# Optimization experiments

Hardware: AMD Instinct MI355X
Metric: run time of the kernel (lower is better)

## Reference

```python
import jax, jax.numpy as jnp
import numpy as np

B, L, H, NUM_VOCABS = 512, 64, 256, 2046
OUT = NUM_VOCABS + 2


def setup_inputs() -> dict:
    key = jax.random.key(0)
    k1, k2, k3 = jax.random.split(key, 3)
    mol_vec = jax.random.normal(k1, (B, L, H), jnp.float32)
    # parent of node t is a strictly earlier node in the same tree; root (t=0) has none
    rng = np.random.default_rng(0)
    pid = np.zeros((B, L), np.int32)
    for t in range(1, L):
        pid[:, t] = rng.integers(0, t, size=B)
    parent_idx = jnp.asarray(pid)
    Wp = jax.random.normal(k2, (H, H), jnp.float32) * (1.0 / np.sqrt(H))
    bp = jnp.zeros((H,), jnp.float32)
    Wc = jax.random.normal(k3, (H, OUT), jnp.float32) * (1.0 / np.sqrt(H))
    bc = jnp.zeros((OUT,), jnp.float32)
    return dict(mol_vec=mol_vec, parent_idx=parent_idx, Wp=Wp, bp=bp, Wc=Wc, bc=bc)


def _sibling_mean(mol_vec, parent_idx):
    # sibling edges connect nodes sharing a parent; message = mean of siblings' mol_vec
    b, l, h = mol_vec.shape
    seg = parent_idx + jnp.arange(b, dtype=parent_idx.dtype)[:, None] * l  # per-tree parent segment
    seg = jnp.where(jnp.arange(l)[None, :] == 0, b * l, seg)  # roots -> dummy segment
    seg_flat = seg.reshape(-1)
    mv_flat = mol_vec.reshape(-1, h)
    child_sum = jax.ops.segment_sum(mv_flat, seg_flat, num_segments=b * l + 1)
    child_cnt = jax.ops.segment_sum(jnp.ones((b * l,), mol_vec.dtype), seg_flat, num_segments=b * l + 1)
    sib_sum = child_sum[seg_flat] - mv_flat           # exclude self
    sib_cnt = child_cnt[seg_flat] - 1.0
    sib_mean = jnp.where(sib_cnt[:, None] > 0, sib_sum / jnp.maximum(sib_cnt, 1.0)[:, None], 0.0)
    sib_mean = sib_mean.reshape(b, l, h)
    # roots receive no sibling update (their dummy segment is meaningless)
    return jnp.where(jnp.arange(l)[None, :, None] == 0, 0.0, sib_mean)


def _forward(mol_vec, parent_idx, Wp, bp, Wc, bc):
    b, l, h = mol_vec.shape
    sib_mean = _sibling_mean(mol_vec, parent_idx)  # static: mol_vec does not depend on z
    batch_ar = jnp.arange(b)

    def body(z, t):
        # gather parent z (each node has exactly one parent edge; sum == gather)
        pz = z[batch_ar, parent_idx[:, t]]                     # [B, H]
        new = jax.nn.relu(pz @ Wp + bp) + sib_mean[:, t]       # parent_layer + sibling mean
        return z.at[:, t].set(new), None

    z0 = jnp.zeros((b, l, h), mol_vec.dtype)
    z, _ = jax.lax.scan(body, z0, jnp.arange(1, l))
    logits = z.reshape(-1, h) @ Wc + bc                         # classify_layer -> [N, V+2]
    return logits


def reference(mol_vec, parent_idx, Wp, bp, Wc, bc):
    return _forward(mol_vec, parent_idx, Wp, bp, Wc, bc)
```

## Files before the change

kernel.cpp:

```cpp
#include <hip/hip_runtime.h>

#define B_ 512
#define L_ 64
#define H_ 256
#define OUT_ 2048

typedef short bf16x8 __attribute__((ext_vector_type(8)));
typedef float f32x4 __attribute__((ext_vector_type(4)));

static __device__ __forceinline__ unsigned short f2bf(float f) {
  union { float f; unsigned int u; } v; v.f = f;
  unsigned int r = (v.u + 0x7FFFu + ((v.u >> 16) & 1u)) >> 16;
  return (unsigned short)r;
}
static __device__ __forceinline__ float bf2f(unsigned short s) {
  union { unsigned int u; float f; } v; v.u = ((unsigned int)s) << 16;
  return v.f;
}

__global__ __launch_bounds__(256) void pack_kernel(
    const float* __restrict__ Wc, const float* __restrict__ Wp,
    unsigned short* __restrict__ WcB, unsigned short* __restrict__ WpB) {
  int bid = blockIdx.x;
  const float* W;
  unsigned short* dst;
  int ncols, col16;
  if (bid < 128) { W = Wc; dst = WcB; ncols = OUT_; col16 = bid; }
  else           { W = Wp; dst = WpB; ncols = H_;   col16 = bid - 128; }
  int tid = threadIdx.x, l = tid & 63, q = tid >> 6;
  int n = col16 * 16 + (l & 15), g = l >> 4;
#pragma unroll
  for (int kk = 0; kk < 2; ++kk) {
    int kt = q + kk * 4;
    bf16x8 v;
#pragma unroll
    for (int i = 0; i < 8; ++i)
      v[i] = (short)f2bf(W[(size_t)(kt * 32 + g * 8 + i) * ncols + n]);
    *(bf16x8*)&dst[(size_t)(col16 * 8 + kt) * 512 + l * 8] = v;
  }
}

__global__ __launch_bounds__(256, 2) void fused_kernel(
    const float* __restrict__ mol, const int* __restrict__ pidx_g,
    const float* __restrict__ bp, const unsigned short* __restrict__ WpB,
    const unsigned short* __restrict__ WcB, const float* __restrict__ bc,
    float* __restrict__ out) {
  __shared__ unsigned short zbuf[65 * H_];
  __shared__ int pidx[L_];
  __shared__ int cnt_i[64];
  __shared__ unsigned short scale_s[64];
  __shared__ int lvlcnt[64];
  __shared__ int lvlbase[64];
  __shared__ int chkbase[64];
  __shared__ int order_s[64];
  __shared__ int cstart_s[64];
  __shared__ int ccnt_s[64];
  __shared__ int nchunks_s;

  int bid = blockIdx.x;
  int b = bid >> 1, half = bid & 1;
  int tid = threadIdx.x;
  int wv = tid >> 6, l = tid & 63, g = l >> 4, c = l & 15;

  if (tid < 64) pidx[tid] = pidx_g[b * L_ + tid];

  const float* molb = mol + (size_t)b * L_ * H_;
#pragma unroll
  for (int i = 0; i < 8; ++i) {
    int idx = tid + i * 256;
    int t = idx >> 5, h0 = (idx & 31) * 8;
    f32x4 lo = *(const f32x4*)&molb[t * H_ + h0];
    f32x4 hi = *(const f32x4*)&molb[t * H_ + h0 + 4];
    bf16x8 v;
#pragma unroll
    for (int q = 0; q < 4; ++q) { v[q] = (short)f2bf(lo[q]); v[q + 4] = (short)f2bf(hi[q]); }
    *(bf16x8*)&zbuf[(t * H_ + h0) ^ ((t & 7) << 3)] = v;
  }

  if (tid < 64) {
    int t = tid;
    cnt_i[t] = 0;
    lvlcnt[t] = 0;
    int pp = pidx[t];
    if (t >= 1) atomicAdd(&cnt_i[pp], 1);
    int lev = (t == 0) ? 0 : 1;
#pragma unroll
    for (int it = 0; it < 6; ++it) {
      int dp = __shfl(lev, pp);
      int pp2 = __shfl(pp, pp);
      lev += dp;
      pp = pp2;
    }
    int cc = (t >= 1) ? (cnt_i[pidx[t]] - 1) : 0;
    scale_s[t] = (t >= 1 && cc > 0) ? f2bf(1.f / (float)cc) : 0;
    int rank = 0;
    if (t >= 1) rank = atomicAdd(&lvlcnt[lev], 1);
    int lc = lvlcnt[t];
    int nchk = (lc + 15) >> 4;
    int offx = lc, chkx = nchk;
#pragma unroll
    for (int d = 1; d < 64; d <<= 1) {
      int u = __shfl_up(offx, d);
      int v2 = __shfl_up(chkx, d);
      if (t >= d) { offx += u; chkx += v2; }
    }
    lvlbase[t] = offx - lc;
    chkbase[t] = chkx - nchk;
    if (t == 63) nchunks_s = chkx;
    if (t >= 1) {
      int pos = lvlbase[lev] + rank;
      order_s[pos] = t;
      if ((rank & 15) == 0) {
        int cid = chkbase[lev] + (rank >> 4);
        cstart_s[cid] = pos;
        ccnt_s[cid] = min(16, lvlcnt[lev] - rank);
      }
    }
  }
  __syncthreads();

  {
    int pv[2][8];
#pragma unroll
    for (int kt = 0; kt < 2; ++kt)
#pragma unroll
      for (int i = 0; i < 8; ++i) pv[kt][i] = pidx[kt * 32 + g * 8 + i];
    bf16x8 bfr[4][2];
#pragma unroll
    for (int nt = 0; nt < 4; ++nt) {
      int tn = nt * 16 + c;
      int pt = pidx[tn];
      unsigned short scl = scale_s[tn];
#pragma unroll
      for (int kt = 0; kt < 2; ++kt) {
        bf16x8 bv;
#pragma unroll
        for (int i = 0; i < 8; ++i) {
          int tp = kt * 32 + g * 8 + i;
          bv[i] = (tp >= 1 && tp != tn && pv[kt][i] == pt) ? (short)scl : (short)0;
        }
        bfr[nt][kt] = bv;
      }
    }
#pragma unroll
    for (int mtl = 0; mtl < 4; ++mtl) {
      int mtg = wv * 4 + mtl;
      int colh = mtg * 16 + c;
      bf16x8 afr[2];
#pragma unroll
      for (int kt = 0; kt < 2; ++kt) {
        bf16x8 av;
#pragma unroll
        for (int i = 0; i < 8; ++i) {
          int tp = kt * 32 + g * 8 + i;
          av[i] = (short)zbuf[(tp * H_ + colh) ^ ((tp & 7) << 3)];
        }
        afr[kt] = av;
      }
      f32x4 acc4[4] = {};
#pragma unroll
      for (int nt = 0; nt < 4; ++nt)
#pragma unroll
        for (int kt = 0; kt < 2; ++kt)
          acc4[nt] = __builtin_amdgcn_mfma_f32_16x16x32_bf16(afr[kt], bfr[nt][kt], acc4[nt], 0, 0, 0);
#pragma unroll
      for (int nt = 0; nt < 4; ++nt) {
        int ts = nt * 16 + c;
        int swn = (ts & 7) << 3;
#pragma unroll
        for (int j = 0; j < 4; ++j) {
          int h = mtg * 16 + g * 4 + j;
          zbuf[(ts * H_ + h) ^ swn] = f2bf(acc4[nt][j]);
        }
      }
    }
  }

  bf16x8 wfr[4][8];
#pragma unroll
  for (int nt = 0; nt < 4; ++nt)
#pragma unroll
    for (int kt = 0; kt < 8; ++kt)
      wfr[nt][kt] = *(const bf16x8*)&WpB[(size_t)((wv * 4 + nt) * 8 + kt) * 512 + l * 8];
  float bpv[4];
#pragma unroll
  for (int nt = 0; nt < 4; ++nt) bpv[nt] = bp[wv * 64 + nt * 16 + c];
  __syncthreads();

  int nch = nchunks_s;
  for (int ch = 0; ch < nch; ++ch) {
    int cs = cstart_s[ch], cc = ccnt_s[ch];
    int node = (c < cc) ? order_s[cs + c] : 64;
    int par = (node < 64) ? pidx[node] : 0;
    int sp = (par & 7) << 3;
    f32x4 a0 = {0.f, 0.f, 0.f, 0.f};
    f32x4 a1 = {0.f, 0.f, 0.f, 0.f};
    f32x4 a2 = {0.f, 0.f, 0.f, 0.f};
    f32x4 a3 = {0.f, 0.f, 0.f, 0.f};
#pragma unroll
    for (int kt = 0; kt < 8; ++kt) {
      bf16x8 av = *(const bf16x8*)&zbuf[par * H_ + ((kt * 32 + g * 8) ^ sp)];
      a0 = __builtin_amdgcn_mfma_f32_16x16x32_bf16(av, wfr[0][kt], a0, 0, 0, 0);
      a1 = __builtin_amdgcn_mfma_f32_16x16x32_bf16(av, wfr[1][kt], a1, 0, 0, 0);
      a2 = __builtin_amdgcn_mfma_f32_16x16x32_bf16(av, wfr[2][kt], a2, 0, 0, 0);
      a3 = __builtin_amdgcn_mfma_f32_16x16x32_bf16(av, wfr[3][kt], a3, 0, 0, 0);
    }
#pragma unroll
    for (int j = 0; j < 4; ++j) {
      int m = g * 4 + j;
      int nd = (m < cc) ? order_s[cs + m] : 64;
      int swn = (nd & 7) << 3;
      int base = nd * H_ + wv * 64 + c;
      int i0 = (base + 0) ^ swn, i1 = (base + 16) ^ swn;
      int i2 = (base + 32) ^ swn, i3 = (base + 48) ^ swn;
      float v0 = fmaxf(a0[j] + bpv[0], 0.f) + bf2f(zbuf[i0]);
      float v1 = fmaxf(a1[j] + bpv[1], 0.f) + bf2f(zbuf[i1]);
      float v2 = fmaxf(a2[j] + bpv[2], 0.f) + bf2f(zbuf[i2]);
      float v3 = fmaxf(a3[j] + bpv[3], 0.f) + bf2f(zbuf[i3]);
      zbuf[i0] = f2bf(v0);
      zbuf[i1] = f2bf(v1);
      zbuf[i2] = f2bf(v2);
      zbuf[i3] = f2bf(v3);
    }
    __syncthreads();
  }

#pragma unroll 1
  for (int nc = 0; nc < 4; ++nc) {
    int colbase = half * 1024 + wv * 256 + nc * 64;
    float bcv[4];
#pragma unroll
    for (int nt = 0; nt < 4; ++nt) bcv[nt] = bc[colbase + nt * 16 + c];
    f32x4 acc[4][4] = {};
#pragma unroll
    for (int kt = 0; kt < 8; ++kt) {
      bf16x8 a[4], bfr[4];
#pragma unroll
      for (int mt = 0; mt < 4; ++mt) {
        int r = mt * 16 + c;
        a[mt] = *(const bf16x8*)&zbuf[r * H_ + ((kt * 32 + g * 8) ^ ((r & 7) << 3))];
      }
#pragma unroll
      for (int nt = 0; nt < 4; ++nt) {
        int col16 = (colbase >> 4) + nt;
        bfr[nt] = *(const bf16x8*)&WcB[(size_t)(col16 * 8 + kt) * 512 + l * 8];
      }
#pragma unroll
      for (int nt = 0; nt < 4; ++nt)
#pragma unroll
        for (int mt = 0; mt < 4; ++mt)
          acc[mt][nt] = __builtin_amdgcn_mfma_f32_16x16x32_bf16(
              a[mt], bfr[nt], acc[mt][nt], 0, 0, 0);
    }
#pragma unroll
    for (int mt = 0; mt < 4; ++mt)
#pragma unroll
      for (int nt = 0; nt < 4; ++nt) {
        int col = colbase + nt * 16 + c;
#pragma unroll
        for (int j = 0; j < 4; ++j) {
          int rt = mt * 16 + g * 4 + j;
          out[(size_t)(b * 64 + rt) * OUT_ + col] = acc[mt][nt][j] + bcv[nt];
        }
      }
  }
}

extern "C" void kernel_launch(void* const* d_in, const int* in_sizes, int n_in,
                              void* d_out, int out_size, void* d_ws, size_t ws_size,
                              hipStream_t stream) {
  const float* mol = (const float*)d_in[0];
  const int* pidx = (const int*)d_in[1];
  const float* Wp = (const float*)d_in[2];
  const float* bp = (const float*)d_in[3];
  const float* Wc = (const float*)d_in[4];
  const float* bc = (const float*)d_in[5];
  float* out = (float*)d_out;

  unsigned short* WcB = (unsigned short*)d_ws;
  unsigned short* WpB = WcB + (size_t)128 * 8 * 512;

  pack_kernel<<<144, 256, 0, stream>>>(Wc, Wp, WcB, WpB);
  fused_kernel<<<2 * B_, 256, 0, stream>>>(mol, pidx, bp, WpB, WcB, bc, out);
}
```

Before: 104.8 us.

## Transpose MFMA operands to vectorize stores and remap block-to-tree order

Swaps the A and B operands of the MFMA calls so each lane holds four consecutive output columns. That lets shared-memory writebacks, the bias loads and the global logits stores become 4-wide vector accesses instead of scalar strided ones. The block index mapping is also changed so the two halves of each tree are launched 8 blocks apart rather than adjacently, which alters scheduling and L2 locality. The risk is the correctness of the transposed fragment indexing in the recurrence update.

```diff
diff --git a/kernel.cpp b/kernel.cpp
--- a/kernel.cpp
+++ b/kernel.cpp
@@ -6,6 +6,7 @@
 #define OUT_ 2048
 
 typedef short bf16x8 __attribute__((ext_vector_type(8)));
+typedef short s16x4 __attribute__((ext_vector_type(4)));
 typedef float f32x4 __attribute__((ext_vector_type(4)));
 
 static __device__ __forceinline__ unsigned short f2bf(float f) {
@@ -58,7 +59,8 @@
   __shared__ int nchunks_s;
 
   int bid = blockIdx.x;
-  int b = bid >> 1, half = bid & 1;
+  int b = ((bid >> 4) << 3) | (bid & 7);
+  int half = (bid >> 3) & 1;
   int tid = threadIdx.x;
   int wv = tid >> 6, l = tid & 63, g = l >> 4, c = l & 15;
 
@@ -166,12 +168,11 @@
 #pragma unroll
       for (int nt = 0; nt < 4; ++nt) {
         int ts = nt * 16 + c;
-        int swn = (ts & 7) << 3;
-#pragma unroll
-        for (int j = 0; j < 4; ++j) {
-          int h = mtg * 16 + g * 4 + j;
-          zbuf[(ts * H_ + h) ^ swn] = f2bf(acc4[nt][j]);
-        }
+        int idx = (ts * H_ + mtg * 16 + g * 4) ^ ((ts & 7) << 3);
+        s16x4 nv;
+#pragma unroll
+        for (int j = 0; j < 4; ++j) nv[j] = (short)f2bf(acc4[nt][j]);
+        *(s16x4*)&zbuf[idx] = nv;
       }
     }
   }
@@ -182,9 +183,10 @@
 #pragma unroll
     for (int kt = 0; kt < 8; ++kt)
       wfr[nt][kt] = *(const bf16x8*)&WpB[(size_t)((wv * 4 + nt) * 8 + kt) * 512 + l * 8];
-  float bpv[4];
-#pragma unroll
-  for (int nt = 0; nt < 4; ++nt) bpv[nt] = bp[wv * 64 + nt * 16 + c];
+  f32x4 bpv4[4];
+#pragma unroll
+  for (int nt = 0; nt < 4; ++nt)
+    bpv4[nt] = *(const f32x4*)&bp[wv * 64 + nt * 16 + g * 4];
   __syncthreads();
 
   int nch = nchunks_s;
@@ -200,27 +202,23 @@
 #pragma unroll
     for (int kt = 0; kt < 8; ++kt) {
       bf16x8 av = *(const bf16x8*)&zbuf[par * H_ + ((kt * 32 + g * 8) ^ sp)];
-      a0 = __builtin_amdgcn_mfma_f32_16x16x32_bf16(av, wfr[0][kt], a0, 0, 0, 0);
-      a1 = __builtin_amdgcn_mfma_f32_16x16x32_bf16(av, wfr[1][kt], a1, 0, 0, 0);
-      a2 = __builtin_amdgcn_mfma_f32_16x16x32_bf16(av, wfr[2][kt], a2, 0, 0, 0);
-      a3 = __builtin_amdgcn_mfma_f32_16x16x32_bf16(av, wfr[3][kt], a3, 0, 0, 0);
-    }
-#pragma unroll
-    for (int j = 0; j < 4; ++j) {
-      int m = g * 4 + j;
-      int nd = (m < cc) ? order_s[cs + m] : 64;
-      int swn = (nd & 7) << 3;
-      int base = nd * H_ + wv * 64 + c;
-      int i0 = (base + 0) ^ swn, i1 = (base + 16) ^ swn;
-      int i2 = (base + 32) ^ swn, i3 = (base + 48) ^ swn;
-      float v0 = fmaxf(a0[j] + bpv[0], 0.f) + bf2f(zbuf[i0]);
-      float v1 = fmaxf(a1[j] + bpv[1], 0.f) + bf2f(zbuf[i1]);
-      float v2 = fmaxf(a2[j] + bpv[2], 0.f) + bf2f(zbuf[i2]);
-      float v3 = fmaxf(a3[j] + bpv[3], 0.f) + bf2f(zbuf[i3]);
-      zbuf[i0] = f2bf(v0);
-      zbuf[i1] = f2bf(v1);
-      zbuf[i2] = f2bf(v2);
-      zbuf[i3] = f2bf(v3);
+      a0 = __builtin_amdgcn_mfma_f32_16x16x32_bf16(wfr[0][kt], av, a0, 0, 0, 0);
+      a1 = __builtin_amdgcn_mfma_f32_16x16x32_bf16(wfr[1][kt], av, a1, 0, 0, 0);
+      a2 = __builtin_amdgcn_mfma_f32_16x16x32_bf16(wfr[2][kt], av, a2, 0, 0, 0);
+      a3 = __builtin_amdgcn_mfma_f32_16x16x32_bf16(wfr[3][kt], av, a3, 0, 0, 0);
+    }
+    int swn = (node & 7) << 3;
+#pragma unroll
+    for (int nt = 0; nt < 4; ++nt) {
+      f32x4 an = (nt == 0) ? a0 : (nt == 1) ? a1 : (nt == 2) ? a2 : a3;
+      int idx = (node * H_ + wv * 64 + nt * 16 + g * 4) ^ swn;
+      s16x4 old = *(const s16x4*)&zbuf[idx];
+      s16x4 nv;
+#pragma unroll
+      for (int j = 0; j < 4; ++j)
+        nv[j] = (short)f2bf(fmaxf(an[j] + bpv4[nt][j], 0.f) +
+                            bf2f((unsigned short)old[j]));
+      *(s16x4*)&zbuf[idx] = nv;
     }
     __syncthreads();
   }
@@ -228,9 +226,10 @@
 #pragma unroll 1
   for (int nc = 0; nc < 4; ++nc) {
     int colbase = half * 1024 + wv * 256 + nc * 64;
-    float bcv[4];
-#pragma unroll
-    for (int nt = 0; nt < 4; ++nt) bcv[nt] = bc[colbase + nt * 16 + c];
+    f32x4 bcv4[4];
+#pragma unroll
+    for (int nt = 0; nt < 4; ++nt)
+      bcv4[nt] = *(const f32x4*)&bc[colbase + nt * 16 + g * 4];
     f32x4 acc[4][4] = {};
 #pragma unroll
     for (int kt = 0; kt < 8; ++kt) {
@@ -250,18 +249,18 @@
 #pragma unroll
         for (int mt = 0; mt < 4; ++mt)
           acc[mt][nt] = __builtin_amdgcn_mfma_f32_16x16x32_bf16(
-              a[mt], bfr[nt], acc[mt][nt], 0, 0, 0);
+              bfr[nt], a[mt], acc[mt][nt], 0, 0, 0);
     }
 #pragma unroll
     for (int mt = 0; mt < 4; ++mt)
 #pragma unroll
       for (int nt = 0; nt < 4; ++nt) {
-        int col = colbase + nt * 16 + c;
-#pragma unroll
-        for (int j = 0; j < 4; ++j) {
-          int rt = mt * 16 + g * 4 + j;
-          out[(size_t)(b * 64 + rt) * OUT_ + col] = acc[mt][nt][j] + bcv[nt];
-        }
+        f32x4 v;
+#pragma unroll
+        for (int j = 0; j < 4; ++j) v[j] = acc[mt][nt][j] + bcv4[nt][j];
+        int row = b * 64 + mt * 16 + c;
+        int col = colbase + nt * 16 + g * 4;
+        *(f32x4*)&out[(size_t)row * OUT_ + col] = v;
       }
   }
 }
```

New measurement: 115.2 us. 1.1x slower.
